# Kernel optimization log

Hardware: AMD Instinct MI355X
Metric: run time of the kernel (lower is better)

The kernel has to match this reference:

```python
import jax, jax.numpy as jnp
import numpy as np

N_ATOMS = 300000
N_BONDS = 600000
MAX_NB = 6
ATOM_FDIM = 133
BOND_FDIM = 147
HIDDEN = 256
DEPTH = 3
N_MOLS = 10000
DIM_TARGET = 1


def setup_inputs() -> dict:
    key = jax.random.key(0)
    ks = jax.random.split(key, 12)
    f_atoms = jax.random.normal(ks[0], (N_ATOMS, ATOM_FDIM), dtype=jnp.float32)
    f_bonds = jax.random.normal(ks[1], (N_BONDS, BOND_FDIM), dtype=jnp.float32)
    a2b = jax.random.randint(ks[2], (N_ATOMS, MAX_NB), 0, N_BONDS, dtype=jnp.int32)
    b2a = jax.random.randint(ks[3], (N_BONDS,), 0, N_ATOMS, dtype=jnp.int32)
    b2revb = jax.random.randint(ks[4], (N_BONDS,), 0, N_BONDS, dtype=jnp.int32)
    segment_ids = jnp.sort(jax.random.randint(ks[5], (N_ATOMS,), 0, N_MOLS, dtype=jnp.int32))
    s = 1.0 / np.sqrt(HIDDEN)
    W_i = jax.random.normal(ks[6], (BOND_FDIM, HIDDEN), dtype=jnp.float32) * s
    W_h = jax.random.normal(ks[7], (HIDDEN, HIDDEN), dtype=jnp.float32) * s
    W_o = jax.random.normal(ks[8], (ATOM_FDIM + HIDDEN, HIDDEN), dtype=jnp.float32) * s
    b_o = jnp.zeros((HIDDEN,), dtype=jnp.float32)
    W_ffn = jax.random.normal(ks[9], (HIDDEN, DIM_TARGET), dtype=jnp.float32) * s
    b_ffn = jnp.zeros((DIM_TARGET,), dtype=jnp.float32)
    return dict(f_atoms=f_atoms, f_bonds=f_bonds, W_i=W_i, W_h=W_h, W_o=W_o,
                b_o=b_o, W_ffn=W_ffn, b_ffn=b_ffn, a2b=a2b, b2a=b2a,
                b2revb=b2revb, segment_ids=segment_ids)


def _mpn_forward(f_atoms, f_bonds, W_i, W_h, W_o, b_o, W_ffn, b_ffn,
                 a2b, b2a, b2revb, segment_ids):
    # input = W_i(f_bonds); message = relu(input)   [n_bonds, H]
    inp = f_bonds @ W_i
    message = jax.nn.relu(inp)
    for _ in range(DEPTH - 1):
        # neighbor gather-sum: [n_atoms, max_nb, H] -> [n_atoms, H]
        a_message = message[a2b].sum(axis=1)
        # bond message = sum over neighbors of source atom minus reverse bond
        message = a_message[b2a] - message[b2revb]
        message = jax.nn.relu(inp + message @ W_h)
    # final atom aggregation
    a_message = message[a2b].sum(axis=1)                      # [n_atoms, H]
    a_input = jnp.concatenate([f_atoms, a_message], axis=1)   # [n_atoms, F+H]
    atom_hiddens = jax.nn.relu(a_input @ W_o + b_o)           # [n_atoms, H]
    # per-molecule mean aggregation (replaces Python narrow+sum loop)
    mol_sum = jax.ops.segment_sum(atom_hiddens, segment_ids, num_segments=N_MOLS)
    counts = jax.ops.segment_sum(jnp.ones((atom_hiddens.shape[0],), atom_hiddens.dtype),
                                 segment_ids, num_segments=N_MOLS)
    mol_vecs = mol_sum / jnp.maximum(counts, 1.0)[:, None]    # zero vec for empty mols
    # MPNN ffn head
    return mol_vecs @ W_ffn + b_ffn                           # [n_mols, dim_target]


def reference(f_atoms, f_bonds, W_i, W_h, W_o, b_o, W_ffn, b_ffn,
              a2b, b2a, b2revb, segment_ids):
    return _mpn_forward(f_atoms, f_bonds, W_i, W_h, W_o, b_o, W_ffn, b_ffn,
                        a2b, b2a, b2revb, segment_ids)
```

## Files before the change

### kernel.cpp

```cpp
#include <hip/hip_runtime.h>

#define NATOMS 300000
#define NBONDS 600000
#define MAXNB  6
#define AFD    133
#define BFD    147
#define HID    256
#define NMOLS  10000

typedef __attribute__((ext_vector_type(8))) short short8;
typedef __attribute__((ext_vector_type(4))) float f32x4;

__device__ __forceinline__ ushort f2bf(float f) {
    union { float f; unsigned u; } x; x.f = f;
    unsigned r = (x.u + 0x7FFFu + ((x.u >> 16) & 1u)) >> 16;
    return (ushort)r;
}
__device__ __forceinline__ float bf2f(ushort h) {
    union { unsigned u; float f; } x; x.u = ((unsigned)h) << 16;
    return x.f;
}

__global__ __launch_bounds__(256) void prep_w(const float* __restrict__ W,
                                              ushort* __restrict__ wt,
                                              int Ksrc, int total, int mode) {
    int gid = blockIdx.x * 256 + threadIdx.x;
    if (gid >= total) return;
    int kl = gid & 63;
    int n  = (gid >> 6) & 255;
    int kc = gid >> 14;
    int k  = kc * 64 + kl;
    float v;
    if (mode == 0) {
        v = (k < Ksrc) ? W[k * 256 + n] : 0.f;
    } else {
        if (k < 192) v = (k < 133) ? W[k * 256 + n] : 0.f;
        else         v = W[(133 + (k - 192)) * 256 + n];
    }
    wt[gid] = f2bf(v);
}

__global__ __launch_bounds__(256) void gather_sum_kernel(const ushort* __restrict__ msg,
                                                         const int* __restrict__ a2b,
                                                         ushort* __restrict__ amsg) {
    int gid = blockIdx.x * 256 + threadIdx.x;
    int a = gid >> 5;
    int coff = (gid & 31) * 8;
    float acc[8] = {0.f,0.f,0.f,0.f,0.f,0.f,0.f,0.f};
    const int* ab = a2b + a * 6;
#pragma unroll
    for (int nb = 0; nb < 6; ++nb) {
        int b = ab[nb];
        union { uint4 u; ushort s[8]; } v;
        v.u = *reinterpret_cast<const uint4*>(msg + (size_t)b * 256 + coff);
#pragma unroll
        for (int j = 0; j < 8; ++j) acc[j] += bf2f(v.s[j]);
    }
    union { uint4 u; ushort s[8]; } o;
#pragma unroll
    for (int j = 0; j < 8; ++j) o.s[j] = f2bf(acc[j]);
    *reinterpret_cast<uint4*>(amsg + (size_t)a * 256 + coff) = o.u;
}

template<int MODE>
__global__ __launch_bounds__(256)
void gemm_kernel(const float* __restrict__ xf,
                 const ushort* __restrict__ amsg,
                 const ushort* __restrict__ msgin,
                 const ushort* __restrict__ inp,
                 const int* __restrict__ b2a,
                 const int* __restrict__ b2revb,
                 const ushort* __restrict__ wt,
                 ushort* __restrict__ out0,
                 ushort* __restrict__ out1,
                 const float* __restrict__ b_o,
                 const float* __restrict__ w_ffn,
                 const int* __restrict__ segids,
                 float* __restrict__ mol_acc,
                 float* __restrict__ mol_cnt,
                 int M, int nchunks)
{
    __shared__ ushort Xs[64 * 72];
    __shared__ ushort Ws[256 * 72];
    __shared__ float rowpart[4][64];
    __shared__ float vals[64];
    __shared__ int   sseg[64];

    const int tid  = threadIdx.x;
    const int wave = tid >> 6;
    const int lane = tid & 63;
    const int q    = lane >> 4;
    const int l16  = lane & 15;
    const int row0 = blockIdx.x * 64;

    const int sr = tid >> 2;
    const int sq = (tid & 3) * 16;

    f32x4 acc[4][4];
#pragma unroll
    for (int i = 0; i < 4; ++i)
#pragma unroll
        for (int j = 0; j < 4; ++j)
            acc[i][j] = (f32x4){0.f, 0.f, 0.f, 0.f};

    int ia = 0, ir = 0;
    if (MODE == 1) { int b = row0 + sr; ia = b2a[b]; ir = b2revb[b]; }

    for (int kc = 0; kc < nchunks; ++kc) {
        {
            const uint4* src = reinterpret_cast<const uint4*>(wt) + (size_t)kc * 2048;
            uint4* dst = reinterpret_cast<uint4*>(Ws);
#pragma unroll
            for (int s = 0; s < 8; ++s) {
                int c = s * 256 + tid;
                dst[(c >> 3) * 9 + (c & 7)] = src[c];
            }
        }
        {
            const int k0 = kc * 64 + sq;
            union { uint4 u[2]; ushort s[16]; } hv;
            if (MODE == 0) {
                int b = row0 + sr;
                const float* p = xf + (size_t)b * BFD;
#pragma unroll
                for (int j = 0; j < 16; ++j) {
                    int k = k0 + j;
                    hv.s[j] = (k < BFD) ? f2bf(p[k]) : (ushort)0;
                }
            } else if (MODE == 1) {
                union { uint4 u[2]; ushort s[16]; } am, mm;
                const uint4* pa = reinterpret_cast<const uint4*>(amsg  + (size_t)ia * 256 + k0);
                const uint4* pm = reinterpret_cast<const uint4*>(msgin + (size_t)ir * 256 + k0);
                am.u[0] = pa[0]; am.u[1] = pa[1];
                mm.u[0] = pm[0]; mm.u[1] = pm[1];
#pragma unroll
                for (int j = 0; j < 16; ++j)
                    hv.s[j] = f2bf(bf2f(am.s[j]) - bf2f(mm.s[j]));
            } else {
                int a = row0 + sr;
                if (a >= M) {
#pragma unroll
                    for (int j = 0; j < 16; ++j) hv.s[j] = 0;
                } else if (k0 >= 192) {
                    const uint4* pa = reinterpret_cast<const uint4*>(amsg + (size_t)a * 256 + (k0 - 192));
                    hv.u[0] = pa[0]; hv.u[1] = pa[1];
                } else {
                    const float* p = xf + (size_t)a * AFD;
#pragma unroll
                    for (int j = 0; j < 16; ++j) {
                        int k = k0 + j;
                        hv.s[j] = (k < AFD) ? f2bf(p[k]) : (ushort)0;
                    }
                }
            }
            uint4* xdst = reinterpret_cast<uint4*>(Xs) + sr * 9 + (tid & 3) * 2;
            xdst[0] = hv.u[0];
            xdst[1] = hv.u[1];
        }
        __syncthreads();

        const uint4* Xs4 = reinterpret_cast<const uint4*>(Xs);
        const uint4* Ws4 = reinterpret_cast<const uint4*>(Ws);
#pragma unroll
        for (int ks = 0; ks < 2; ++ks) {
            short8 af[4], bfr[4];
#pragma unroll
            for (int mt = 0; mt < 4; ++mt) {
                union { uint4 u; short8 s; } t;
                t.u = Xs4[(mt * 16 + l16) * 9 + ks * 4 + q];
                af[mt] = t.s;
            }
#pragma unroll
            for (int nt = 0; nt < 4; ++nt) {
                int n = wave * 64 + nt * 16 + l16;
                union { uint4 u; short8 s; } t;
                t.u = Ws4[n * 9 + ks * 4 + q];
                bfr[nt] = t.s;
            }
#pragma unroll
            for (int mt = 0; mt < 4; ++mt)
#pragma unroll
                for (int nt = 0; nt < 4; ++nt)
                    acc[mt][nt] = __builtin_amdgcn_mfma_f32_16x16x32_bf16(
                        af[mt], bfr[nt], acc[mt][nt], 0, 0, 0);
        }
        __syncthreads();
    }

    if (MODE == 0) {
#pragma unroll
        for (int mt = 0; mt < 4; ++mt)
#pragma unroll
            for (int rr = 0; rr < 4; ++rr) {
                int grow = row0 + mt * 16 + q * 4 + rr;
#pragma unroll
                for (int nt = 0; nt < 4; ++nt) {
                    int gcol = wave * 64 + nt * 16 + l16;
                    size_t idx = (size_t)grow * 256 + gcol;
                    float v = acc[mt][nt][rr];
                    out0[idx] = f2bf(v);
                    out1[idx] = f2bf(fmaxf(v, 0.f));
                }
            }
    } else if (MODE == 1) {
#pragma unroll
        for (int mt = 0; mt < 4; ++mt)
#pragma unroll
            for (int rr = 0; rr < 4; ++rr) {
                int grow = row0 + mt * 16 + q * 4 + rr;
#pragma unroll
                for (int nt = 0; nt < 4; ++nt) {
                    int gcol = wave * 64 + nt * 16 + l16;
                    size_t idx = (size_t)grow * 256 + gcol;
                    float v = acc[mt][nt][rr] + bf2f(inp[idx]);
                    out0[idx] = f2bf(fmaxf(v, 0.f));
                }
            }
    } else {
        float bo4[4], wf4[4];
#pragma unroll
        for (int nt = 0; nt < 4; ++nt) {
            int gcol = wave * 64 + nt * 16 + l16;
            bo4[nt] = b_o[gcol];
            wf4[nt] = w_ffn[gcol];
        }
#pragma unroll
        for (int mt = 0; mt < 4; ++mt)
#pragma unroll
            for (int rr = 0; rr < 4; ++rr) {
                float s = 0.f;
#pragma unroll
                for (int nt = 0; nt < 4; ++nt) {
                    float h = fmaxf(acc[mt][nt][rr] + bo4[nt], 0.f);
                    s = fmaf(h, wf4[nt], s);
                }
#pragma unroll
                for (int off = 1; off < 16; off <<= 1)
                    s += __shfl_xor(s, off, 64);
                if (l16 == 0) rowpart[wave][mt * 16 + q * 4 + rr] = s;
            }
        __syncthreads();
        if (tid < 64) {
            int a = row0 + tid;
            vals[tid] = rowpart[0][tid] + rowpart[1][tid] + rowpart[2][tid] + rowpart[3][tid];
            sseg[tid] = (a < M) ? segids[a] : -1;
        }
        __syncthreads();
        if (tid < 64) {
            int myseg = sseg[tid];
            bool leader = (myseg >= 0) && (tid == 0 || sseg[tid - 1] != myseg);
            if (leader) {
                float sum = 0.f; int cnt = 0;
                for (int rr = tid; rr < 64 && sseg[rr] == myseg; ++rr) { sum += vals[rr]; ++cnt; }
                atomicAdd(mol_acc + myseg, sum);
                atomicAdd(mol_cnt + myseg, (float)cnt);
            }
        }
    }
}

__global__ __launch_bounds__(256) void finalize_kernel(const float* __restrict__ mol_acc,
                                                       const float* __restrict__ mol_cnt,
                                                       const float* __restrict__ b_ffn,
                                                       float* __restrict__ out) {
    int m = blockIdx.x * 256 + threadIdx.x;
    if (m < NMOLS)
        out[m] = mol_acc[m] / fmaxf(mol_cnt[m], 1.f) + b_ffn[0];
}

extern "C" void kernel_launch(void* const* d_in, const int* in_sizes, int n_in,
                              void* d_out, int out_size, void* d_ws, size_t ws_size,
                              hipStream_t stream) {
    const float* f_atoms = (const float*)d_in[0];
    const float* f_bonds = (const float*)d_in[1];
    const float* W_i     = (const float*)d_in[2];
    const float* W_h     = (const float*)d_in[3];
    const float* W_o     = (const float*)d_in[4];
    const float* b_o     = (const float*)d_in[5];
    const float* W_ffn   = (const float*)d_in[6];
    const float* b_ffn   = (const float*)d_in[7];
    const int* a2b       = (const int*)d_in[8];
    const int* b2a       = (const int*)d_in[9];
    const int* b2revb    = (const int*)d_in[10];
    const int* segids    = (const int*)d_in[11];
    float* out = (float*)d_out;

    char* ws = (char*)d_ws;
    size_t off = 0;
    ushort* inp  = (ushort*)(ws + off); off += (size_t)NBONDS * 256 * 2;
    ushort* msgA = (ushort*)(ws + off); off += (size_t)NBONDS * 256 * 2;
    ushort* msgB = (ushort*)(ws + off); off += (size_t)NBONDS * 256 * 2;
    ushort* amsg = (ushort*)(ws + off); off += (size_t)NATOMS * 256 * 2;
    ushort* wi_t = (ushort*)(ws + off); off += (size_t)192 * 256 * 2;
    ushort* wh_t = (ushort*)(ws + off); off += (size_t)256 * 256 * 2;
    ushort* wo_t = (ushort*)(ws + off); off += (size_t)448 * 256 * 2;
    float* mol_acc = (float*)(ws + off); off += (size_t)NMOLS * 4;
    float* mol_cnt = (float*)(ws + off); off += (size_t)NMOLS * 4;

    prep_w<<<(192 * 256 + 255) / 256, 256, 0, stream>>>(W_i, wi_t, BFD, 192 * 256, 0);
    prep_w<<<(256 * 256 + 255) / 256, 256, 0, stream>>>(W_h, wh_t, 256, 256 * 256, 0);
    prep_w<<<(448 * 256 + 255) / 256, 256, 0, stream>>>(W_o, wo_t, 133, 448 * 256, 1);

    gemm_kernel<0><<<NBONDS / 64, 256, 0, stream>>>(
        f_bonds, nullptr, nullptr, nullptr, nullptr, nullptr, wi_t,
        inp, msgA, nullptr, nullptr, nullptr, nullptr, nullptr, NBONDS, 3);

    ushort* cur = msgA; ushort* nxt = msgB;
    for (int d = 0; d < 2; ++d) {
        gather_sum_kernel<<<NATOMS * 32 / 256, 256, 0, stream>>>(cur, a2b, amsg);
        gemm_kernel<1><<<NBONDS / 64, 256, 0, stream>>>(
            nullptr, amsg, cur, inp, b2a, b2revb, wh_t,
            nxt, nullptr, nullptr, nullptr, nullptr, nullptr, nullptr, NBONDS, 4);
        ushort* t = cur; cur = nxt; nxt = t;
    }
    gather_sum_kernel<<<NATOMS * 32 / 256, 256, 0, stream>>>(cur, a2b, amsg);

    hipMemsetAsync(mol_acc, 0, (size_t)NMOLS * 2 * 4, stream);

    gemm_kernel<2><<<(NATOMS + 63) / 64, 256, 0, stream>>>(
        f_atoms, amsg, nullptr, nullptr, nullptr, nullptr, wo_t,
        nullptr, nullptr, b_o, W_ffn, segids, mol_acc, mol_cnt, NATOMS, 7);

    finalize_kernel<<<(NMOLS + 255) / 256, 256, 0, stream>>>(mol_acc, mol_cnt, b_ffn, out);
}
```

Measured before the change: 2.309 ms.

## Rewrite GEMMs to load pre-swizzled MFMA fragments directly, dropping LDS staging

Weights are pre-packed into MFMA fragment order, so each wave loads its B fragments straight from global memory (L2-resident) and builds A fragments directly from gathered rows, with no shared-memory staging and no barriers. Each wave now owns 64 rows by 128 columns, and the grid is split into two column halves, so A rows are loaded twice. The first GEMM stores only the pre-activation, and ReLU is applied on the fly in the gather and in the first message step, which removes one full bond-sized write. The risk is heavier global and L2 traffic from per-wave fragment loads and higher register pressure from the 4x8 accumulator tile.

```diff
diff --git a/kernel.cpp b/kernel.cpp
--- a/kernel.cpp
+++ b/kernel.cpp
@@ -2,10 +2,8 @@
 
 #define NATOMS 300000
 #define NBONDS 600000
-#define MAXNB  6
 #define AFD    133
 #define BFD    147
-#define HID    256
 #define NMOLS  10000
 
 typedef __attribute__((ext_vector_type(8))) short short8;
@@ -20,26 +18,42 @@
     union { unsigned u; float f; } x; x.u = ((unsigned)h) << 16;
     return x.f;
 }
-
-__global__ __launch_bounds__(256) void prep_w(const float* __restrict__ W,
-                                              ushort* __restrict__ wt,
-                                              int Ksrc, int total, int mode) {
+__device__ __forceinline__ unsigned pack_bf(float f0, float f1) {
+    return __builtin_amdgcn_perm(__float_as_uint(f1), __float_as_uint(f0), 0x07060302u);
+}
+template<bool RELUM>
+__device__ __forceinline__ unsigned bfpair_sub(unsigned a, unsigned m) {
+    float al = __uint_as_float(a << 16), ah = __uint_as_float(a & 0xFFFF0000u);
+    float ml = __uint_as_float(m << 16), mh = __uint_as_float(m & 0xFFFF0000u);
+    if (RELUM) { ml = fmaxf(ml, 0.f); mh = fmaxf(mh, 0.f); }
+    return pack_bf(al - ml, ah - mh);
+}
+
+__global__ __launch_bounds__(256) void prep_w2(const float* __restrict__ W,
+                                               ushort* __restrict__ wt,
+                                               int KS, int Ksrc, int mode) {
     int gid = blockIdx.x * 256 + threadIdx.x;
-    if (gid >= total) return;
-    int kl = gid & 63;
-    int n  = (gid >> 6) & 255;
-    int kc = gid >> 14;
-    int k  = kc * 64 + kl;
-    float v;
-    if (mode == 0) {
-        v = (k < Ksrc) ? W[k * 256 + n] : 0.f;
-    } else {
-        if (k < 192) v = (k < 133) ? W[k * 256 + n] : 0.f;
-        else         v = W[(133 + (k - 192)) * 256 + n];
-    }
-    wt[gid] = f2bf(v);
-}
-
+    if (gid >= KS * 1024) return;
+    int lane = gid & 63;
+    int ncb  = (gid >> 6) & 15;
+    int ks   = gid >> 10;
+    int n  = ncb * 16 + (lane & 15);
+    int k0 = ks * 32 + (lane >> 4) * 8;
+#pragma unroll
+    for (int j = 0; j < 8; ++j) {
+        int k = k0 + j;
+        float v;
+        if (mode == 0) {
+            v = (k < Ksrc) ? W[k * 256 + n] : 0.f;
+        } else {
+            if (k < 192) v = (k < 133) ? W[k * 256 + n] : 0.f;
+            else         v = W[(133 + (k - 192)) * 256 + n];
+        }
+        wt[(size_t)gid * 8 + j] = f2bf(v);
+    }
+}
+
+template<bool RELU>
 __global__ __launch_bounds__(256) void gather_sum_kernel(const ushort* __restrict__ msg,
                                                          const int* __restrict__ a2b,
                                                          ushort* __restrict__ amsg) {
@@ -54,7 +68,11 @@
         union { uint4 u; ushort s[8]; } v;
         v.u = *reinterpret_cast<const uint4*>(msg + (size_t)b * 256 + coff);
 #pragma unroll
-        for (int j = 0; j < 8; ++j) acc[j] += bf2f(v.s[j]);
+        for (int j = 0; j < 8; ++j) {
+            float t = bf2f(v.s[j]);
+            if (RELU) t = fmaxf(t, 0.f);
+            acc[j] += t;
+        }
     }
     union { uint4 u; ushort s[8]; } o;
 #pragma unroll
@@ -62,167 +80,135 @@
     *reinterpret_cast<uint4*>(amsg + (size_t)a * 256 + coff) = o.u;
 }
 
-template<int MODE>
-__global__ __launch_bounds__(256)
-void gemm_kernel(const float* __restrict__ xf,
-                 const ushort* __restrict__ amsg,
-                 const ushort* __restrict__ msgin,
-                 const ushort* __restrict__ inp,
-                 const int* __restrict__ b2a,
-                 const int* __restrict__ b2revb,
-                 const ushort* __restrict__ wt,
-                 ushort* __restrict__ out0,
-                 ushort* __restrict__ out1,
-                 const float* __restrict__ b_o,
-                 const float* __restrict__ w_ffn,
-                 const int* __restrict__ segids,
-                 float* __restrict__ mol_acc,
-                 float* __restrict__ mol_cnt,
-                 int M, int nchunks)
+template<int MODE, bool RELUSRC>
+__global__ __launch_bounds__(256, 2)
+void gemm_v2(const float* __restrict__ xf,
+             const ushort* __restrict__ amsg,
+             const ushort* __restrict__ msgin,
+             const ushort* __restrict__ inp,
+             const int* __restrict__ b2a,
+             const int* __restrict__ b2revb,
+             const ushort* __restrict__ wt,
+             ushort* __restrict__ out0,
+             const float* __restrict__ b_o,
+             const float* __restrict__ w_ffn,
+             const int* __restrict__ segids,
+             float* __restrict__ mol_acc,
+             float* __restrict__ mol_cnt,
+             int M)
 {
-    __shared__ ushort Xs[64 * 72];
-    __shared__ ushort Ws[256 * 72];
-    __shared__ float rowpart[4][64];
-    __shared__ float vals[64];
-    __shared__ int   sseg[64];
+    __shared__ float svals[4][64];
+    __shared__ int   sseg[4][64];
 
     const int tid  = threadIdx.x;
     const int wave = tid >> 6;
     const int lane = tid & 63;
     const int q    = lane >> 4;
     const int l16  = lane & 15;
-    const int row0 = blockIdx.x * 64;
-
-    const int sr = tid >> 2;
-    const int sq = (tid & 3) * 16;
-
-    f32x4 acc[4][4];
+    const int half = blockIdx.x;
+    const int rb   = blockIdx.y;
+    const int rowbase = rb * 256 + wave * 64;
+    const int colbase = half * 128;
+
+    f32x4 acc[4][8];
 #pragma unroll
     for (int i = 0; i < 4; ++i)
 #pragma unroll
-        for (int j = 0; j < 4; ++j)
-            acc[i][j] = (f32x4){0.f, 0.f, 0.f, 0.f};
-
-    int ia = 0, ir = 0;
-    if (MODE == 1) { int b = row0 + sr; ia = b2a[b]; ir = b2revb[b]; }
-
-    for (int kc = 0; kc < nchunks; ++kc) {
-        {
-            const uint4* src = reinterpret_cast<const uint4*>(wt) + (size_t)kc * 2048;
-            uint4* dst = reinterpret_cast<uint4*>(Ws);
-#pragma unroll
-            for (int s = 0; s < 8; ++s) {
-                int c = s * 256 + tid;
-                dst[(c >> 3) * 9 + (c & 7)] = src[c];
-            }
-        }
-        {
-            const int k0 = kc * 64 + sq;
-            union { uint4 u[2]; ushort s[16]; } hv;
-            if (MODE == 0) {
-                int b = row0 + sr;
-                const float* p = xf + (size_t)b * BFD;
-#pragma unroll
-                for (int j = 0; j < 16; ++j) {
-                    int k = k0 + j;
-                    hv.s[j] = (k < BFD) ? f2bf(p[k]) : (ushort)0;
+        for (int j = 0; j < 8; ++j)
+            acc[i][j] = (f32x4){0.f,0.f,0.f,0.f};
+
+    int rc[4], ia[4], ir[4];
+#pragma unroll
+    for (int mt = 0; mt < 4; ++mt) {
+        int r = rowbase + mt * 16 + l16;
+        rc[mt] = (r < M) ? r : (M - 1);
+        if (MODE == 1) { ia[mt] = b2a[rc[mt]]; ir[mt] = b2revb[rc[mt]]; }
+    }
+
+    constexpr int NKS = (MODE == 0) ? 5 : (MODE == 1 ? 8 : 14);
+
+#pragma unroll
+    for (int ks = 0; ks < NKS; ++ks) {
+        if (MODE == 2 && ks == 5) continue;
+
+        union { uint4 u; short8 s; } bfr[8];
+#pragma unroll
+        for (int nt = 0; nt < 8; ++nt) {
+            int ncb = half * 8 + nt;
+            bfr[nt].u = *reinterpret_cast<const uint4*>(wt + ((size_t)(ks * 16 + ncb) * 64 + lane) * 8);
+        }
+
+        union { uint4 u; short8 s; } afr[4];
+#pragma unroll
+        for (int mt = 0; mt < 4; ++mt) {
+            if (MODE == 1) {
+                uint4 a = *reinterpret_cast<const uint4*>(amsg  + (size_t)ia[mt] * 256 + ks * 32 + q * 8);
+                uint4 m = *reinterpret_cast<const uint4*>(msgin + (size_t)ir[mt] * 256 + ks * 32 + q * 8);
+                afr[mt].u.x = bfpair_sub<RELUSRC>(a.x, m.x);
+                afr[mt].u.y = bfpair_sub<RELUSRC>(a.y, m.y);
+                afr[mt].u.z = bfpair_sub<RELUSRC>(a.z, m.z);
+                afr[mt].u.w = bfpair_sub<RELUSRC>(a.w, m.w);
+            } else if (MODE == 2 && ks >= 6) {
+                afr[mt].u = *reinterpret_cast<const uint4*>(amsg + (size_t)rc[mt] * 256 + (ks - 6) * 32 + q * 8);
+            } else {
+                const int FD = (MODE == 0) ? BFD : AFD;
+                const float* p = xf + (size_t)rc[mt] * FD + ks * 32 + q * 8;
+                float v[8];
+#pragma unroll
+                for (int j = 0; j < 8; ++j) {
+                    int k = ks * 32 + q * 8 + j;
+                    v[j] = (k < FD) ? p[j] : 0.f;
                 }
-            } else if (MODE == 1) {
-                union { uint4 u[2]; ushort s[16]; } am, mm;
-                const uint4* pa = reinterpret_cast<const uint4*>(amsg  + (size_t)ia * 256 + k0);
-                const uint4* pm = reinterpret_cast<const uint4*>(msgin + (size_t)ir * 256 + k0);
-                am.u[0] = pa[0]; am.u[1] = pa[1];
-                mm.u[0] = pm[0]; mm.u[1] = pm[1];
-#pragma unroll
-                for (int j = 0; j < 16; ++j)
-                    hv.s[j] = f2bf(bf2f(am.s[j]) - bf2f(mm.s[j]));
-            } else {
-                int a = row0 + sr;
-                if (a >= M) {
-#pragma unroll
-                    for (int j = 0; j < 16; ++j) hv.s[j] = 0;
-                } else if (k0 >= 192) {
-                    const uint4* pa = reinterpret_cast<const uint4*>(amsg + (size_t)a * 256 + (k0 - 192));
-                    hv.u[0] = pa[0]; hv.u[1] = pa[1];
-                } else {
-                    const float* p = xf + (size_t)a * AFD;
-#pragma unroll
-                    for (int j = 0; j < 16; ++j) {
-                        int k = k0 + j;
-                        hv.s[j] = (k < AFD) ? f2bf(p[k]) : (ushort)0;
-                    }
+                afr[mt].u.x = pack_bf(v[0], v[1]);
+                afr[mt].u.y = pack_bf(v[2], v[3]);
+                afr[mt].u.z = pack_bf(v[4], v[5]);
+                afr[mt].u.w = pack_bf(v[6], v[7]);
+            }
+        }
+
+#pragma unroll
+        for (int mt = 0; mt < 4; ++mt)
+#pragma unroll
+            for (int nt = 0; nt < 8; ++nt)
+                acc[mt][nt] = __builtin_amdgcn_mfma_f32_16x16x32_bf16(
+                    afr[mt].s, bfr[nt].s, acc[mt][nt], 0, 0, 0);
+    }
+
+    if (MODE == 0) {
+#pragma unroll
+        for (int mt = 0; mt < 4; ++mt)
+#pragma unroll
+            for (int rr = 0; rr < 4; ++rr) {
+                int grow = rowbase + mt * 16 + q * 4 + rr;
+                if (grow >= M) continue;
+#pragma unroll
+                for (int nt = 0; nt < 8; ++nt) {
+                    int gcol = colbase + nt * 16 + l16;
+                    out0[(size_t)grow * 256 + gcol] = f2bf(acc[mt][nt][rr]);
                 }
             }
-            uint4* xdst = reinterpret_cast<uint4*>(Xs) + sr * 9 + (tid & 3) * 2;
-            xdst[0] = hv.u[0];
-            xdst[1] = hv.u[1];
-        }
-        __syncthreads();
-
-        const uint4* Xs4 = reinterpret_cast<const uint4*>(Xs);
-        const uint4* Ws4 = reinterpret_cast<const uint4*>(Ws);
-#pragma unroll
-        for (int ks = 0; ks < 2; ++ks) {
-            short8 af[4], bfr[4];
-#pragma unroll
-            for (int mt = 0; mt < 4; ++mt) {
-                union { uint4 u; short8 s; } t;
-                t.u = Xs4[(mt * 16 + l16) * 9 + ks * 4 + q];
-                af[mt] = t.s;
-            }
-#pragma unroll
-            for (int nt = 0; nt < 4; ++nt) {
-                int n = wave * 64 + nt * 16 + l16;
-                union { uint4 u; short8 s; } t;
-                t.u = Ws4[n * 9 + ks * 4 + q];
-                bfr[nt] = t.s;
-            }
-#pragma unroll
-            for (int mt = 0; mt < 4; ++mt)
-#pragma unroll
-                for (int nt = 0; nt < 4; ++nt)
-                    acc[mt][nt] = __builtin_amdgcn_mfma_f32_16x16x32_bf16(
-                        af[mt], bfr[nt], acc[mt][nt], 0, 0, 0);
-        }
-        __syncthreads();
-    }
-
-    if (MODE == 0) {
+    } else if (MODE == 1) {
 #pragma unroll
         for (int mt = 0; mt < 4; ++mt)
 #pragma unroll
             for (int rr = 0; rr < 4; ++rr) {
-                int grow = row0 + mt * 16 + q * 4 + rr;
-#pragma unroll
-                for (int nt = 0; nt < 4; ++nt) {
-                    int gcol = wave * 64 + nt * 16 + l16;
-                    size_t idx = (size_t)grow * 256 + gcol;
-                    float v = acc[mt][nt][rr];
-                    out0[idx] = f2bf(v);
-                    out1[idx] = f2bf(fmaxf(v, 0.f));
-                }
-            }
-    } else if (MODE == 1) {
-#pragma unroll
-        for (int mt = 0; mt < 4; ++mt)
-#pragma unroll
-            for (int rr = 0; rr < 4; ++rr) {
-                int grow = row0 + mt * 16 + q * 4 + rr;
-#pragma unroll
-                for (int nt = 0; nt < 4; ++nt) {
-                    int gcol = wave * 64 + nt * 16 + l16;
+                int grow = rowbase + mt * 16 + q * 4 + rr;
+                if (grow >= M) continue;
+#pragma unroll
+                for (int nt = 0; nt < 8; ++nt) {
+                    int gcol = colbase + nt * 16 + l16;
                     size_t idx = (size_t)grow * 256 + gcol;
                     float v = acc[mt][nt][rr] + bf2f(inp[idx]);
                     out0[idx] = f2bf(fmaxf(v, 0.f));
                 }
             }
     } else {
-        float bo4[4], wf4[4];
-#pragma unroll
-        for (int nt = 0; nt < 4; ++nt) {
-            int gcol = wave * 64 + nt * 16 + l16;
-            bo4[nt] = b_o[gcol];
-            wf4[nt] = w_ffn[gcol];
+        float bo[8], wf[8];
+#pragma unroll
+        for (int nt = 0; nt < 8; ++nt) {
+            int gcol = colbase + nt * 16 + l16;
+            bo[nt] = b_o[gcol];
+            wf[nt] = w_ffn[gcol];
         }
 #pragma unroll
         for (int mt = 0; mt < 4; ++mt)
@@ -230,30 +216,30 @@
             for (int rr = 0; rr < 4; ++rr) {
                 float s = 0.f;
 #pragma unroll
-                for (int nt = 0; nt < 4; ++nt) {
-                    float h = fmaxf(acc[mt][nt][rr] + bo4[nt], 0.f);
-                    s = fmaf(h, wf4[nt], s);
+                for (int nt = 0; nt < 8; ++nt) {
+                    float h = fmaxf(acc[mt][nt][rr] + bo[nt], 0.f);
+                    s = fmaf(h, wf[nt], s);
                 }
 #pragma unroll
                 for (int off = 1; off < 16; off <<= 1)
                     s += __shfl_xor(s, off, 64);
-                if (l16 == 0) rowpart[wave][mt * 16 + q * 4 + rr] = s;
-            }
+                if (l16 == 0) svals[wave][mt * 16 + q * 4 + rr] = s;
+            }
+        {
+            int rl = lane;
+            int grow = rb * 256 + wave * 64 + rl;
+            sseg[wave][rl] = (grow < M) ? segids[grow] : -1;
+        }
         __syncthreads();
-        if (tid < 64) {
-            int a = row0 + tid;
-            vals[tid] = rowpart[0][tid] + rowpart[1][tid] + rowpart[2][tid] + rowpart[3][tid];
-            sseg[tid] = (a < M) ? segids[a] : -1;
-        }
-        __syncthreads();
-        if (tid < 64) {
-            int myseg = sseg[tid];
-            bool leader = (myseg >= 0) && (tid == 0 || sseg[tid - 1] != myseg);
+        {
+            int w = tid >> 6, rl = tid & 63;
+            int myseg = sseg[w][rl];
+            bool leader = (myseg >= 0) && (rl == 0 || sseg[w][rl - 1] != myseg);
             if (leader) {
                 float sum = 0.f; int cnt = 0;
-                for (int rr = tid; rr < 64 && sseg[rr] == myseg; ++rr) { sum += vals[rr]; ++cnt; }
+                for (int j = rl; j < 64 && sseg[w][j] == myseg; ++j) { sum += svals[w][j]; ++cnt; }
                 atomicAdd(mol_acc + myseg, sum);
-                atomicAdd(mol_cnt + myseg, (float)cnt);
+                if (half == 0) atomicAdd(mol_cnt + myseg, (float)cnt);
             }
         }
     }
@@ -287,39 +273,41 @@
 
     char* ws = (char*)d_ws;
     size_t off = 0;
-    ushort* inp  = (ushort*)(ws + off); off += (size_t)NBONDS * 256 * 2;
-    ushort* msgA = (ushort*)(ws + off); off += (size_t)NBONDS * 256 * 2;
-    ushort* msgB = (ushort*)(ws + off); off += (size_t)NBONDS * 256 * 2;
+    ushort* inp  = (ushort*)(ws + off); off += (size_t)600064 * 256 * 2;
+    ushort* msg1 = (ushort*)(ws + off); off += (size_t)600064 * 256 * 2;
+    ushort* msg2 = (ushort*)(ws + off); off += (size_t)600064 * 256 * 2;
     ushort* amsg = (ushort*)(ws + off); off += (size_t)NATOMS * 256 * 2;
-    ushort* wi_t = (ushort*)(ws + off); off += (size_t)192 * 256 * 2;
-    ushort* wh_t = (ushort*)(ws + off); off += (size_t)256 * 256 * 2;
-    ushort* wo_t = (ushort*)(ws + off); off += (size_t)448 * 256 * 2;
+    ushort* wi_t = (ushort*)(ws + off); off += (size_t)5  * 1024 * 8 * 2;
+    ushort* wh_t = (ushort*)(ws + off); off += (size_t)8  * 1024 * 8 * 2;
+    ushort* wo_t = (ushort*)(ws + off); off += (size_t)14 * 1024 * 8 * 2;
     float* mol_acc = (float*)(ws + off); off += (size_t)NMOLS * 4;
     float* mol_cnt = (float*)(ws + off); off += (size_t)NMOLS * 4;
 
-    prep_w<<<(192 * 256 + 255) / 256, 256, 0, stream>>>(W_i, wi_t, BFD, 192 * 256, 0);
-    prep_w<<<(256 * 256 + 255) / 256, 256, 0, stream>>>(W_h, wh_t, 256, 256 * 256, 0);
-    prep_w<<<(448 * 256 + 255) / 256, 256, 0, stream>>>(W_o, wo_t, 133, 448 * 256, 1);
-
-    gemm_kernel<0><<<NBONDS / 64, 256, 0, stream>>>(
+    prep_w2<<<(5  * 1024 + 255) / 256, 256, 0, stream>>>(W_i, wi_t, 5,  BFD, 0);
+    prep_w2<<<(8  * 1024 + 255) / 256, 256, 0, stream>>>(W_h, wh_t, 8,  256, 0);
+    prep_w2<<<(14 * 1024 + 255) / 256, 256, 0, stream>>>(W_o, wo_t, 14, 133, 1);
+
+    gemm_v2<0, false><<<dim3(2, 2344), 256, 0, stream>>>(
         f_bonds, nullptr, nullptr, nullptr, nullptr, nullptr, wi_t,
-        inp, msgA, nullptr, nullptr, nullptr, nullptr, nullptr, NBONDS, 3);
-
-    ushort* cur = msgA; ushort* nxt = msgB;
-    for (int d = 0; d < 2; ++d) {
-        gather_sum_kernel<<<NATOMS * 32 / 256, 256, 0, stream>>>(cur, a2b, amsg);
-        gemm_kernel<1><<<NBONDS / 64, 256, 0, stream>>>(
-            nullptr, amsg, cur, inp, b2a, b2revb, wh_t,
-            nxt, nullptr, nullptr, nullptr, nullptr, nullptr, nullptr, NBONDS, 4);
-        ushort* t = cur; cur = nxt; nxt = t;
-    }
-    gather_sum_kernel<<<NATOMS * 32 / 256, 256, 0, stream>>>(cur, a2b, amsg);
+        inp, nullptr, nullptr, nullptr, nullptr, nullptr, NBONDS);
+
+    gather_sum_kernel<true><<<NATOMS * 32 / 256, 256, 0, stream>>>(inp, a2b, amsg);
+    gemm_v2<1, true><<<dim3(2, 2344), 256, 0, stream>>>(
+        nullptr, amsg, inp, inp, b2a, b2revb, wh_t,
+        msg1, nullptr, nullptr, nullptr, nullptr, nullptr, NBONDS);
+
+    gather_sum_kernel<false><<<NATOMS * 32 / 256, 256, 0, stream>>>(msg1, a2b, amsg);
+    gemm_v2<1, false><<<dim3(2, 2344), 256, 0, stream>>>(
+        nullptr, amsg, msg1, inp, b2a, b2revb, wh_t,
+        msg2, nullptr, nullptr, nullptr, nullptr, nullptr, NBONDS);
+
+    gather_sum_kernel<false><<<NATOMS * 32 / 256, 256, 0, stream>>>(msg2, a2b, amsg);
 
     hipMemsetAsync(mol_acc, 0, (size_t)NMOLS * 2 * 4, stream);
 
-    gemm_kernel<2><<<(NATOMS + 63) / 64, 256, 0, stream>>>(
+    gemm_v2<2, false><<<dim3(2, 1172), 256, 0, stream>>>(
         f_atoms, amsg, nullptr, nullptr, nullptr, nullptr, wo_t,
-        nullptr, nullptr, b_o, W_ffn, segids, mol_acc, mol_cnt, NATOMS, 7);
+        nullptr, b_o, W_ffn, segids, mol_acc, mol_cnt, NATOMS);
 
     finalize_kernel<<<(NMOLS + 255) / 256, 256, 0, stream>>>(mol_acc, mol_cnt, b_ffn, out);
 }
```

Measured after the change: 2.156 ms. -6.7%, faster.
